# Kernel optimization log

Measured on AMD Instinct MI355X. Metric: run time of the kernel, lower is better.

Reference implementation:

```python
import jax, jax.numpy as jnp
import numpy as np

N_NODES = 100000


def _gcn_layer(x, W, b, src, dst, deg_inv_sqrt):
    # x: [N, Din] -> [N, Dout]; PyG GCNConv: linear, then normalized sum-aggregate
    xw = x @ W                                   # [N, Dout]
    norm = deg_inv_sqrt[src] * deg_inv_sqrt[dst]  # [Eh]
    msg = xw[src] * norm[:, None]                # gather + scale, [Eh, Dout]
    out = jax.ops.segment_sum(msg, dst, num_segments=N_NODES)
    return out + b


def reference(x, edge_index, W1, b1, W2, b2):
    N = N_NODES
    # add self-loops once; reused by both layers (same graph)
    loops = jnp.arange(N, dtype=edge_index.dtype)
    src = jnp.concatenate([edge_index[0], loops])  # row
    dst = jnp.concatenate([edge_index[1], loops])  # col
    # degree of destination (col) with unit edge weights, incl. self loops
    deg = jax.ops.segment_sum(jnp.ones_like(src, dtype=x.dtype), dst, num_segments=N)
    deg_inv_sqrt = jnp.where(deg > 0, jax.lax.rsqrt(deg), 0.0)

    h = _gcn_layer(x, W1, b1, src, dst, deg_inv_sqrt)
    h = jax.nn.relu(h)
    out = _gcn_layer(h, W2, b2, src, dst, deg_inv_sqrt)
    return out


def setup_inputs() -> dict:
    key = jax.random.key(0)
    k1, k2, k3, k4 = jax.random.split(key, 4)
    N, E, IN, HID, OUT = N_NODES, 1600000, 128, 64, 64
    x = jax.random.normal(k1, (N, IN), dtype=jnp.float32)
    edge_index = jax.random.randint(k2, (2, E), 0, N, dtype=jnp.int64)
    # Glorot-ish scaled weights
    W1 = jax.random.normal(k3, (IN, HID), dtype=jnp.float32) * (1.0 / np.sqrt(IN))
    W2 = jax.random.normal(k4, (HID, OUT), dtype=jnp.float32) * (1.0 / np.sqrt(HID))
    b1 = jnp.zeros((HID,), dtype=jnp.float32)
    b2 = jnp.zeros((OUT,), dtype=jnp.float32)
    return {"x": x, "edge_index": edge_index, "W1": W1, "b1": b1, "W2": W2, "b2": b2}
```

## Files before the change

### kernel.cpp

```cpp
#include <hip/hip_runtime.h>
#include <hip/hip_bf16.h>
#include <hip/hip_fp16.h>


#define IN_DIM 128
#define HID 64
#define SUB 8
#define CAPS 256
#define CURPAD 16
#define BENT (SUB * CAPS)

__global__ __launch_bounds__(256) void fill_kernel(
    const int* __restrict__ src, const int* __restrict__ dst,
    int* __restrict__ bcur, int* __restrict__ ents, int E) {
  int e = blockIdx.x * 256 + threadIdx.x;
  if (e >= E) return;
  int s = src[e], d = dst[e];
  int seg = (d >> 6) * SUB + (blockIdx.x & 7);
  int pos = atomicAdd(&bcur[seg * CURPAD], 1);
  if (pos < CAPS) ents[(size_t)seg * CAPS + pos] = (s << 6) | (d & 63);
}

__global__ __launch_bounds__(256) void sort_kernel(
    const int* __restrict__ ents, const int* __restrict__ bcur,
    int* __restrict__ csr, int* __restrict__ start_, int* __restrict__ end_,
    float* __restrict__ dinv, int N) {
  __shared__ int stage[BENT];
  __shared__ int sorted[BENT];
  __shared__ int scnt[SUB], soff[SUB + 1];
  __shared__ int hist[64], cur[64];
  int b = blockIdx.x, tid = threadIdx.x;
  int base = b * BENT;

  if (tid < SUB) {
    int c = bcur[(b * SUB + tid) * CURPAD];
    scnt[tid] = c < CAPS ? c : CAPS;
  }
  if (tid < 64) hist[tid] = 0;
  __syncthreads();
  if (tid == 0) {
    int a = 0;
#pragma unroll
    for (int i = 0; i < SUB; ++i) { soff[i] = a; a += scnt[i]; }
    soff[SUB] = a;
  }
  __syncthreads();
  int total = soff[SUB];

#pragma unroll
  for (int i = 0; i < SUB; ++i) {
    const int* ep = ents + (size_t)(b * SUB + i) * CAPS;
    for (int j = tid; j < scnt[i]; j += 256) stage[soff[i] + j] = ep[j];
  }
  __syncthreads();

  for (int j = tid; j < total; j += 256) atomicAdd(&hist[stage[j] & 63], 1);
  __syncthreads();

  if (tid < 64) {
    int c = hist[tid];
    int x = c;
#pragma unroll
    for (int off = 1; off < 64; off <<= 1) {
      int t = __shfl_up(x, off);
      if (tid >= off) x += t;
    }
    int excl = x - c;
    cur[tid] = excl;
    int r = b * 64 + tid;
    if (r < N) {
      start_[r] = base + excl;
      end_[r] = base + excl + c;
      dinv[r] = rsqrtf((float)(c + 1));
    }
  }
  __syncthreads();

  for (int j = tid; j < total; j += 256) {
    int e = stage[j];
    int p = atomicAdd(&cur[e & 63], 1);
    sorted[p] = e >> 6;
  }
  __syncthreads();

  for (int j = tid; j < total; j += 256) csr[base + j] = sorted[j];
}

__global__ __launch_bounds__(256) void gemm1_kernel(
    const float* __restrict__ x, const float* __restrict__ W1,
    const float* __restrict__ dinv, __half* __restrict__ y1, int N) {
  __shared__ float Xs[IN_DIM][68];
  __shared__ float Ws[IN_DIM * HID];

  for (int i = threadIdx.x; i < IN_DIM * HID / 4; i += 256)
    ((float4*)Ws)[i] = ((const float4*)W1)[i];

  int r0 = blockIdx.x * 64;
  {
    int row = threadIdx.x >> 2;
    int kc = (threadIdx.x & 3) * 32;
    int gr = r0 + row;
    const float* xp = x + (size_t)(gr < N ? gr : N - 1) * IN_DIM + kc;
#pragma unroll
    for (int i = 0; i < 8; ++i) {
      float4 v = *(const float4*)(xp + i * 4);
      int k = kc + i * 4;
      Xs[k + 0][row] = v.x;
      Xs[k + 1][row] = v.y;
      Xs[k + 2][row] = v.z;
      Xs[k + 3][row] = v.w;
    }
  }
  __syncthreads();

  int tr = (threadIdx.x & 15) * 4;
  int tc = (threadIdx.x >> 4) * 4;
  float acc[4][4];
#pragma unroll
  for (int i = 0; i < 4; ++i)
#pragma unroll
    for (int j = 0; j < 4; ++j) acc[i][j] = 0.f;

#pragma unroll 8
  for (int k = 0; k < IN_DIM; ++k) {
    float4 a = *(const float4*)&Xs[k][tr];
    float4 bb = *(const float4*)&Ws[k * HID + tc];
    acc[0][0] = fmaf(a.x, bb.x, acc[0][0]); acc[0][1] = fmaf(a.x, bb.y, acc[0][1]);
    acc[0][2] = fmaf(a.x, bb.z, acc[0][2]); acc[0][3] = fmaf(a.x, bb.w, acc[0][3]);
    acc[1][0] = fmaf(a.y, bb.x, acc[1][0]); acc[1][1] = fmaf(a.y, bb.y, acc[1][1]);
    acc[1][2] = fmaf(a.y, bb.z, acc[1][2]); acc[1][3] = fmaf(a.y, bb.w, acc[1][3]);
    acc[2][0] = fmaf(a.z, bb.x, acc[2][0]); acc[2][1] = fmaf(a.z, bb.y, acc[2][1]);
    acc[2][2] = fmaf(a.z, bb.z, acc[2][2]); acc[2][3] = fmaf(a.z, bb.w, acc[2][3]);
    acc[3][0] = fmaf(a.w, bb.x, acc[3][0]); acc[3][1] = fmaf(a.w, bb.y, acc[3][1]);
    acc[3][2] = fmaf(a.w, bb.z, acc[3][2]); acc[3][3] = fmaf(a.w, bb.w, acc[3][3]);
  }

#pragma unroll
  for (int i = 0; i < 4; ++i) {
    int r = r0 + tr + i;
    if (r < N) {
      float di = dinv[r];
      ushort4 w;
      w.x = __half_as_ushort(__float2half(acc[i][0] * di));
      w.y = __half_as_ushort(__float2half(acc[i][1] * di));
      w.z = __half_as_ushort(__float2half(acc[i][2] * di));
      w.w = __half_as_ushort(__float2half(acc[i][3] * di));
      *(ushort4*)(y1 + ((size_t)r << 6) + tc) = w;
    }
  }
}

#define GSTEP(U, A) { unsigned o = ((unsigned)__shfl(idx, i + U) << 6) | lane; \
                      A += __half2float(y[o]); }
__device__ __forceinline__ float gather_row(
    const __half* __restrict__ y, int idx, int m, unsigned lane) {
  float a0 = 0.f, a1 = 0.f, a2 = 0.f, a3 = 0.f;
  float a4 = 0.f, a5 = 0.f, a6 = 0.f, a7 = 0.f;
  float a8 = 0.f, a9 = 0.f, a10 = 0.f, a11 = 0.f;
  float a12 = 0.f, a13 = 0.f, a14 = 0.f, a15 = 0.f;
  int i = 0;
  for (; i + 15 < m; i += 16) {
    GSTEP(0, a0)  GSTEP(1, a1)  GSTEP(2, a2)  GSTEP(3, a3)
    GSTEP(4, a4)  GSTEP(5, a5)  GSTEP(6, a6)  GSTEP(7, a7)
    GSTEP(8, a8)  GSTEP(9, a9)  GSTEP(10, a10) GSTEP(11, a11)
    GSTEP(12, a12) GSTEP(13, a13) GSTEP(14, a14) GSTEP(15, a15)
  }
  if (i + 7 < m) {
    GSTEP(0, a0) GSTEP(1, a1) GSTEP(2, a2) GSTEP(3, a3)
    GSTEP(4, a4) GSTEP(5, a5) GSTEP(6, a6) GSTEP(7, a7)
    i += 8;
  }
  if (i + 3 < m) {
    GSTEP(0, a8) GSTEP(1, a9) GSTEP(2, a10) GSTEP(3, a11)
    i += 4;
  }
  for (; i < m; ++i) GSTEP(0, a12)
  return (((a0 + a1) + (a2 + a3)) + ((a4 + a5) + (a6 + a7))) +
         (((a8 + a9) + (a10 + a11)) + ((a12 + a13) + (a14 + a15)));
}
#undef GSTEP

__global__ __launch_bounds__(256) void agg1_gemm2_kernel(
    const __half* __restrict__ y1, const int* __restrict__ start_,
    const int* __restrict__ end_, const int* __restrict__ csr,
    const float* __restrict__ dinv, const float* __restrict__ b1,
    const float* __restrict__ W2, __half* __restrict__ y2, int N) {
  __shared__ float Ws[HID * HID];
  __shared__ float hs[4][HID];
  for (int i = threadIdx.x; i < HID * HID / 4; i += 256)
    ((float4*)Ws)[i] = ((const float4*)W2)[i];
  __syncthreads();

  int wave = threadIdx.x >> 6;
  unsigned lane = threadIdx.x & 63;
  int r = blockIdx.x * 4 + wave;
  bool valid = r < N;
  int rr = valid ? r : N - 1;

  int jb = start_[rr], je = end_[rr];
  int cnt = je - jb;
  int m = cnt < 64 ? cnt : 64;
  int idx = ((int)lane < cnt) ? csr[jb + lane] : 0;

  float acc = __half2float(y1[((unsigned)rr << 6) | lane]);
  acc += gather_row(y1, idx, m, lane);
  for (int j = jb + 64; j < je; ++j)
    acc += __half2float(y1[((unsigned)csr[j] << 6) | lane]);

  float di = dinv[rr];
  hs[wave][lane] = fmaxf(fmaf(acc, di, b1[lane]), 0.f);

  float c0 = 0.f, c1 = 0.f, c2 = 0.f, c3 = 0.f;
#pragma unroll
  for (int k = 0; k < HID; k += 4) {
    float4 hv = *(const float4*)&hs[wave][k];
    c0 = fmaf(hv.x, Ws[(k + 0) * HID + lane], c0);
    c1 = fmaf(hv.y, Ws[(k + 1) * HID + lane], c1);
    c2 = fmaf(hv.z, Ws[(k + 2) * HID + lane], c2);
    c3 = fmaf(hv.w, Ws[(k + 3) * HID + lane], c3);
  }
  if (valid)
    y2[((unsigned)r << 6) | lane] = __float2half(((c0 + c1) + (c2 + c3)) * di);
}

__global__ __launch_bounds__(256) void agg2_kernel(
    const __half* __restrict__ y2, const int* __restrict__ start_,
    const int* __restrict__ end_, const int* __restrict__ csr,
    const float* __restrict__ dinv, const float* __restrict__ b2,
    float* __restrict__ out, int N) {
  int wave = threadIdx.x >> 6;
  unsigned lane = threadIdx.x & 63;
  int r = blockIdx.x * 4 + wave;
  if (r >= N) return;

  int jb = start_[r], je = end_[r];
  int cnt = je - jb;
  int m = cnt < 64 ? cnt : 64;
  int idx = ((int)lane < cnt) ? csr[jb + lane] : 0;

  float acc = __half2float(y2[((unsigned)r << 6) | lane]);
  acc += gather_row(y2, idx, m, lane);
  for (int j = jb + 64; j < je; ++j)
    acc += __half2float(y2[((unsigned)csr[j] << 6) | lane]);

  out[((unsigned)r << 6) | lane] = fmaf(acc, dinv[r], b2[lane]);
}

extern "C" void kernel_launch(void* const* d_in, const int* in_sizes, int n_in,
                              void* d_out, int out_size, void* d_ws, size_t ws_size,
                              hipStream_t stream) {
  const float* x   = (const float*)d_in[0];
  const int* edges = (const int*)d_in[1];
  const float* W1  = (const float*)d_in[2];
  const float* b1  = (const float*)d_in[3];
  const float* W2  = (const float*)d_in[4];
  const float* b2  = (const float*)d_in[5];
  float* out = (float*)d_out;

  const int N = in_sizes[0] / IN_DIM;
  const int E = in_sizes[1] / 2;
  const int* src = edges;
  const int* dst = edges + E;
  const int NBUCK = (N + 63) / 64;

  char* wsb = (char*)d_ws;
  float*  dinv   = (float*)(wsb + 0);
  int*    start_ = (int*)(wsb + (size_t)512 * 1024);
  int*    end_   = (int*)(wsb + (size_t)1024 * 1024);
  int*    bcur   = (int*)(wsb + (size_t)1536 * 1024);
  int*    ents   = (int*)(wsb + (size_t)3 * 1024 * 1024);
  int*    csr    = ents;
  __half* y1     = (__half*)(wsb + (size_t)16 * 1024 * 1024);
  __half* y2     = (__half*)(wsb + (size_t)30 * 1024 * 1024);

  const int blk = 256;
  int gE = (E + blk - 1) / blk;
  int gG = (N + 63) / 64;
  int gR = (N + 3) / 4;

  hipMemsetAsync(bcur, 0, (size_t)NBUCK * SUB * CURPAD * 4, stream);
  fill_kernel<<<gE, blk, 0, stream>>>(src, dst, bcur, ents, E);
  sort_kernel<<<NBUCK, blk, 0, stream>>>(ents, bcur, csr, start_, end_, dinv, N);

  gemm1_kernel<<<gG, blk, 0, stream>>>(x, W1, dinv, y1, N);
  agg1_gemm2_kernel<<<gR, blk, 0, stream>>>(y1, start_, end_, csr, dinv, b1, W2, y2, N);
  agg2_kernel<<<gR, blk, 0, stream>>>(y2, start_, end_, csr, dinv, b2, out, N);
}
```

Measured before the change: 260.8 us.

## Aggregate two rows per wave with branchless batched gathers via zero row

Each wave now aggregates two destination rows, the second taken from the other half of the node range, so each wave has twice as many independent loads in flight. Neighbour gathers are issued in fixed batches of 16 per row. Slots past the real neighbour count are redirected to a zero padding row at index N, so the gather loop has no data-dependent branches. The change adds a tiny kernel to zero that padding row. It costs extra wasted loads for low-degree rows and higher register pressure, which may reduce occupancy.

```diff
diff --git a/kernel.cpp b/kernel.cpp
--- a/kernel.cpp
+++ b/kernel.cpp
@@ -86,6 +86,12 @@
   for (int j = tid; j < total; j += 256) csr[base + j] = sorted[j];
 }
 
+__global__ void zrow_kernel(__half* __restrict__ y1, __half* __restrict__ y2, int N) {
+  int lane = threadIdx.x;
+  y1[((size_t)N << 6) + lane] = __float2half(0.f);
+  y2[((size_t)N << 6) + lane] = __float2half(0.f);
+}
+
 __global__ __launch_bounds__(256) void gemm1_kernel(
     const float* __restrict__ x, const float* __restrict__ W1,
     const float* __restrict__ dinv, __half* __restrict__ y1, int N) {
@@ -150,100 +156,151 @@
   }
 }
 
-#define GSTEP(U, A) { unsigned o = ((unsigned)__shfl(idx, i + U) << 6) | lane; \
-                      A += __half2float(y[o]); }
-__device__ __forceinline__ float gather_row(
-    const __half* __restrict__ y, int idx, int m, unsigned lane) {
+__device__ __forceinline__ void batch32_pair(
+    const __half* __restrict__ y, int idxA, int mA, int idxB, int mB,
+    int zrow, unsigned lane, float& accA_o, float& accB_o) {
+  ushort v[32];
+#pragma unroll
+  for (int u = 0; u < 16; ++u) {
+    int s = __shfl(idxA, u);
+    s = (u < mA) ? s : zrow;
+    v[u] = ((const ushort*)y)[((unsigned)s << 6) | lane];
+  }
+#pragma unroll
+  for (int u = 0; u < 16; ++u) {
+    int s = __shfl(idxB, u);
+    s = (u < mB) ? s : zrow;
+    v[16 + u] = ((const ushort*)y)[((unsigned)s << 6) | lane];
+  }
   float a0 = 0.f, a1 = 0.f, a2 = 0.f, a3 = 0.f;
-  float a4 = 0.f, a5 = 0.f, a6 = 0.f, a7 = 0.f;
-  float a8 = 0.f, a9 = 0.f, a10 = 0.f, a11 = 0.f;
-  float a12 = 0.f, a13 = 0.f, a14 = 0.f, a15 = 0.f;
-  int i = 0;
-  for (; i + 15 < m; i += 16) {
-    GSTEP(0, a0)  GSTEP(1, a1)  GSTEP(2, a2)  GSTEP(3, a3)
-    GSTEP(4, a4)  GSTEP(5, a5)  GSTEP(6, a6)  GSTEP(7, a7)
-    GSTEP(8, a8)  GSTEP(9, a9)  GSTEP(10, a10) GSTEP(11, a11)
-    GSTEP(12, a12) GSTEP(13, a13) GSTEP(14, a14) GSTEP(15, a15)
-  }
-  if (i + 7 < m) {
-    GSTEP(0, a0) GSTEP(1, a1) GSTEP(2, a2) GSTEP(3, a3)
-    GSTEP(4, a4) GSTEP(5, a5) GSTEP(6, a6) GSTEP(7, a7)
-    i += 8;
-  }
-  if (i + 3 < m) {
-    GSTEP(0, a8) GSTEP(1, a9) GSTEP(2, a10) GSTEP(3, a11)
-    i += 4;
-  }
-  for (; i < m; ++i) GSTEP(0, a12)
-  return (((a0 + a1) + (a2 + a3)) + ((a4 + a5) + (a6 + a7))) +
-         (((a8 + a9) + (a10 + a11)) + ((a12 + a13) + (a14 + a15)));
-}
-#undef GSTEP
+  float b0 = 0.f, b1 = 0.f, b2 = 0.f, b3 = 0.f;
+#pragma unroll
+  for (int u = 0; u < 16; u += 4) {
+    a0 += __half2float(__ushort_as_half(v[u + 0]));
+    a1 += __half2float(__ushort_as_half(v[u + 1]));
+    a2 += __half2float(__ushort_as_half(v[u + 2]));
+    a3 += __half2float(__ushort_as_half(v[u + 3]));
+    b0 += __half2float(__ushort_as_half(v[16 + u + 0]));
+    b1 += __half2float(__ushort_as_half(v[16 + u + 1]));
+    b2 += __half2float(__ushort_as_half(v[16 + u + 2]));
+    b3 += __half2float(__ushort_as_half(v[16 + u + 3]));
+  }
+  accA_o = (a0 + a1) + (a2 + a3);
+  accB_o = (b0 + b1) + (b2 + b3);
+}
+
+__device__ __forceinline__ float batch16_tail(
+    const __half* __restrict__ y, int idx, int i0, int m, int zrow,
+    unsigned lane) {
+  ushort v[16];
+#pragma unroll
+  for (int u = 0; u < 16; ++u) {
+    int s = __shfl(idx, i0 + u);
+    s = (i0 + u < m) ? s : zrow;
+    v[u] = ((const ushort*)y)[((unsigned)s << 6) | lane];
+  }
+  float a0 = 0.f, a1 = 0.f, a2 = 0.f, a3 = 0.f;
+#pragma unroll
+  for (int u = 0; u < 16; u += 4) {
+    a0 += __half2float(__ushort_as_half(v[u + 0]));
+    a1 += __half2float(__ushort_as_half(v[u + 1]));
+    a2 += __half2float(__ushort_as_half(v[u + 2]));
+    a3 += __half2float(__ushort_as_half(v[u + 3]));
+  }
+  return (a0 + a1) + (a2 + a3);
+}
+
+__device__ __forceinline__ void agg_two_rows(
+    const __half* __restrict__ y, const int* __restrict__ start_,
+    const int* __restrict__ end_, const int* __restrict__ csr,
+    int rrA, int rrB, int zrow, unsigned lane, float& accA, float& accB) {
+  int jbA = start_[rrA], jeA = end_[rrA];
+  int jbB = start_[rrB], jeB = end_[rrB];
+  int cntA = jeA - jbA, cntB = jeB - jbB;
+  int idxA = ((int)lane < cntA) ? csr[jbA + lane] : zrow;
+  int idxB = ((int)lane < cntB) ? csr[jbB + lane] : zrow;
+  int mA = cntA < 64 ? cntA : 64;
+  int mB = cntB < 64 ? cntB : 64;
+
+  float aA, aB;
+  batch32_pair(y, idxA, mA < 16 ? mA : 16, idxB, mB < 16 ? mB : 16,
+               zrow, lane, aA, aB);
+  accA = aA + __half2float(y[((unsigned)rrA << 6) | lane]);
+  accB = aB + __half2float(y[((unsigned)rrB << 6) | lane]);
+  for (int i = 16; i < mA; i += 16)
+    accA += batch16_tail(y, idxA, i, mA, zrow, lane);
+  for (int i = 16; i < mB; i += 16)
+    accB += batch16_tail(y, idxB, i, mB, zrow, lane);
+  for (int j = jbA + 64; j < jeA; ++j)
+    accA += __half2float(y[((unsigned)csr[j] << 6) | lane]);
+  for (int j = jbB + 64; j < jeB; ++j)
+    accB += __half2float(y[((unsigned)csr[j] << 6) | lane]);
+}
 
 __global__ __launch_bounds__(256) void agg1_gemm2_kernel(
     const __half* __restrict__ y1, const int* __restrict__ start_,
     const int* __restrict__ end_, const int* __restrict__ csr,
     const float* __restrict__ dinv, const float* __restrict__ b1,
-    const float* __restrict__ W2, __half* __restrict__ y2, int N) {
+    const float* __restrict__ W2, __half* __restrict__ y2, int N, int halfN) {
   __shared__ float Ws[HID * HID];
-  __shared__ float hs[4][HID];
+  __shared__ float hs[8][HID];
   for (int i = threadIdx.x; i < HID * HID / 4; i += 256)
     ((float4*)Ws)[i] = ((const float4*)W2)[i];
   __syncthreads();
 
   int wave = threadIdx.x >> 6;
   unsigned lane = threadIdx.x & 63;
-  int r = blockIdx.x * 4 + wave;
-  bool valid = r < N;
-  int rr = valid ? r : N - 1;
-
-  int jb = start_[rr], je = end_[rr];
-  int cnt = je - jb;
-  int m = cnt < 64 ? cnt : 64;
-  int idx = ((int)lane < cnt) ? csr[jb + lane] : 0;
-
-  float acc = __half2float(y1[((unsigned)rr << 6) | lane]);
-  acc += gather_row(y1, idx, m, lane);
-  for (int j = jb + 64; j < je; ++j)
-    acc += __half2float(y1[((unsigned)csr[j] << 6) | lane]);
-
-  float di = dinv[rr];
-  hs[wave][lane] = fmaxf(fmaf(acc, di, b1[lane]), 0.f);
-
-  float c0 = 0.f, c1 = 0.f, c2 = 0.f, c3 = 0.f;
+  int rA = blockIdx.x * 4 + wave;
+  int rB = rA + halfN;
+  bool vA = rA < N, vB = rB < N;
+  int rrA = vA ? rA : N - 1;
+  int rrB = vB ? rB : N - 1;
+
+  float accA, accB;
+  agg_two_rows(y1, start_, end_, csr, rrA, rrB, N, lane, accA, accB);
+
+  float diA = dinv[rrA], diB = dinv[rrB];
+  hs[wave][lane]     = fmaxf(fmaf(accA, diA, b1[lane]), 0.f);
+  hs[wave + 4][lane] = fmaxf(fmaf(accB, diB, b1[lane]), 0.f);
+
+  float cA0 = 0.f, cA1 = 0.f, cA2 = 0.f, cA3 = 0.f;
+  float cB0 = 0.f, cB1 = 0.f, cB2 = 0.f, cB3 = 0.f;
 #pragma unroll
   for (int k = 0; k < HID; k += 4) {
-    float4 hv = *(const float4*)&hs[wave][k];
-    c0 = fmaf(hv.x, Ws[(k + 0) * HID + lane], c0);
-    c1 = fmaf(hv.y, Ws[(k + 1) * HID + lane], c1);
-    c2 = fmaf(hv.z, Ws[(k + 2) * HID + lane], c2);
-    c3 = fmaf(hv.w, Ws[(k + 3) * HID + lane], c3);
-  }
-  if (valid)
-    y2[((unsigned)r << 6) | lane] = __float2half(((c0 + c1) + (c2 + c3)) * di);
+    float4 hA = *(const float4*)&hs[wave][k];
+    float4 hB = *(const float4*)&hs[wave + 4][k];
+    float w0 = Ws[(k + 0) * HID + lane], w1 = Ws[(k + 1) * HID + lane];
+    float w2 = Ws[(k + 2) * HID + lane], w3 = Ws[(k + 3) * HID + lane];
+    cA0 = fmaf(hA.x, w0, cA0); cA1 = fmaf(hA.y, w1, cA1);
+    cA2 = fmaf(hA.z, w2, cA2); cA3 = fmaf(hA.w, w3, cA3);
+    cB0 = fmaf(hB.x, w0, cB0); cB1 = fmaf(hB.y, w1, cB1);
+    cB2 = fmaf(hB.z, w2, cB2); cB3 = fmaf(hB.w, w3, cB3);
+  }
+  if (vA)
+    y2[((unsigned)rA << 6) | lane] = __float2half(((cA0 + cA1) + (cA2 + cA3)) * diA);
+  if (vB)
+    y2[((unsigned)rB << 6) | lane] = __float2half(((cB0 + cB1) + (cB2 + cB3)) * diB);
 }
 
 __global__ __launch_bounds__(256) void agg2_kernel(
     const __half* __restrict__ y2, const int* __restrict__ start_,
     const int* __restrict__ end_, const int* __restrict__ csr,
     const float* __restrict__ dinv, const float* __restrict__ b2,
-    float* __restrict__ out, int N) {
+    float* __restrict__ out, int N, int halfN) {
   int wave = threadIdx.x >> 6;
   unsigned lane = threadIdx.x & 63;
-  int r = blockIdx.x * 4 + wave;
-  if (r >= N) return;
-
-  int jb = start_[r], je = end_[r];
-  int cnt = je - jb;
-  int m = cnt < 64 ? cnt : 64;
-  int idx = ((int)lane < cnt) ? csr[jb + lane] : 0;
-
-  float acc = __half2float(y2[((unsigned)r << 6) | lane]);
-  acc += gather_row(y2, idx, m, lane);
-  for (int j = jb + 64; j < je; ++j)
-    acc += __half2float(y2[((unsigned)csr[j] << 6) | lane]);
-
-  out[((unsigned)r << 6) | lane] = fmaf(acc, dinv[r], b2[lane]);
+  int rA = blockIdx.x * 4 + wave;
+  int rB = rA + halfN;
+  bool vA = rA < N, vB = rB < N;
+  int rrA = vA ? rA : N - 1;
+  int rrB = vB ? rB : N - 1;
+
+  float accA, accB;
+  agg_two_rows(y2, start_, end_, csr, rrA, rrB, N, lane, accA, accB);
+
+  float bv = b2[lane];
+  if (vA) out[((unsigned)rA << 6) | lane] = fmaf(accA, dinv[rrA], bv);
+  if (vB) out[((unsigned)rB << 6) | lane] = fmaf(accB, dinv[rrB], bv);
 }
 
 extern "C" void kernel_launch(void* const* d_in, const int* in_sizes, int n_in,
@@ -262,6 +319,7 @@
   const int* src = edges;
   const int* dst = edges + E;
   const int NBUCK = (N + 63) / 64;
+  const int halfN = (N + 1) / 2;
 
   char* wsb = (char*)d_ws;
   float*  dinv   = (float*)(wsb + 0);
@@ -276,13 +334,14 @@
   const int blk = 256;
   int gE = (E + blk - 1) / blk;
   int gG = (N + 63) / 64;
-  int gR = (N + 3) / 4;
+  int gR2 = (halfN + 3) / 4;
 
   hipMemsetAsync(bcur, 0, (size_t)NBUCK * SUB * CURPAD * 4, stream);
   fill_kernel<<<gE, blk, 0, stream>>>(src, dst, bcur, ents, E);
   sort_kernel<<<NBUCK, blk, 0, stream>>>(ents, bcur, csr, start_, end_, dinv, N);
+  zrow_kernel<<<1, 64, 0, stream>>>(y1, y2, N);
 
   gemm1_kernel<<<gG, blk, 0, stream>>>(x, W1, dinv, y1, N);
-  agg1_gemm2_kernel<<<gR, blk, 0, stream>>>(y1, start_, end_, csr, dinv, b1, W2, y2, N);
-  agg2_kernel<<<gR, blk, 0, stream>>>(y2, start_, end_, csr, dinv, b2, out, N);
-}
+  agg1_gemm2_kernel<<<gR2, blk, 0, stream>>>(y1, start_, end_, csr, dinv, b1, W2, y2, N, halfN);
+  agg2_kernel<<<gR2, blk, 0, stream>>>(y2, start_, end_, csr, dinv, b2, out, N, halfN);
+}
```

New measurement: 275.3 us. +5.6%, slower.
